# Kernel tuning notes

Hardware: AMD Instinct MI355X
Metric: run time of the kernel (lower is better)

## Reference

```python
import jax, jax.numpy as jnp
import numpy as np

IN_FEATURES = 1024
NUM_EXPERTS = 64
TOP_K = 2


def setup_inputs() -> dict:
    key = jax.random.key(0)
    kx, kw, kb = jax.random.split(key, 3)
    x = jax.random.normal(kx, (8, 4096, IN_FEATURES), dtype=jnp.float32)
    # nn.Linear init scale ~ 1/sqrt(in_features)
    bound = 1.0 / np.sqrt(IN_FEATURES)
    W = jax.random.uniform(kw, (NUM_EXPERTS, IN_FEATURES), dtype=jnp.float32, minval=-bound, maxval=bound)
    b = jax.random.uniform(kb, (NUM_EXPERTS,), dtype=jnp.float32, minval=-bound, maxval=bound)
    return {"x": x, "W": W, "b": b}


def reference(x, W, b):
    # logits: [B, S, E]
    logits = jnp.einsum("bsd,ed->bse", x, W) + b
    gates = jax.nn.softmax(logits, axis=-1)
    top_k_gates, top_k_indices = jax.lax.top_k(gates, TOP_K)
    return top_k_gates, top_k_indices
```

## Files before the change

### kernel.cpp

```cpp
#include <hip/hip_runtime.h>
#include <hip/hip_bf16.h>

#define D 1024
#define E 64
#define TPB 256
#define TOKS 64
#define KC 64
#define NCHUNK (D / KC)

typedef __attribute__((ext_vector_type(8))) short bf16x8;
typedef __attribute__((ext_vector_type(4))) float f32x4;
typedef __attribute__((ext_vector_type(4))) int i32x4;
typedef __attribute__((ext_vector_type(4))) unsigned short u16x4;

__device__ __forceinline__ unsigned short bf16_rne(float f) {
    unsigned u = __builtin_bit_cast(unsigned, f);
    u += 0x7fffu + ((u >> 16) & 1u);
    return (unsigned short)(u >> 16);
}
__device__ __forceinline__ float bf16_as_f(unsigned short h) {
    unsigned u = ((unsigned)h) << 16;
    return __builtin_bit_cast(float, u);
}
__device__ __forceinline__ void split_hi_lo(float v, unsigned short& h, unsigned short& l) {
    h = bf16_rne(v);
    l = bf16_rne(v - bf16_as_f(h));
}

__global__ __launch_bounds__(256) void wsplit_kernel(const float* __restrict__ W,
        unsigned short* __restrict__ whi, unsigned short* __restrict__ wlo) {
    int g = blockIdx.x * 256 + threadIdx.x;
    f32x4 w = *(const f32x4*)(W + (size_t)g * 4);
    u16x4 h, l;
#pragma unroll
    for (int j = 0; j < 4; ++j) {
        unsigned short hh, ll;
        split_hi_lo(w[j], hh, ll);
        h[j] = hh; l[j] = ll;
    }
    *(u16x4*)(whi + (size_t)g * 4) = h;
    *(u16x4*)(wlo + (size_t)g * 4) = l;
}

__global__ __launch_bounds__(TPB, 2) void router_kernel(
        const float* __restrict__ x,
        const unsigned short* __restrict__ whi,
        const unsigned short* __restrict__ wlo,
        const float* __restrict__ bias,
        float* __restrict__ out, int T) {
    __shared__ float ls[TOKS][E + 1];

    const int tid  = threadIdx.x;
    const int lane = tid & 63;
    const int wid  = tid >> 6;
    const int n    = lane & 15;
    const int q    = lane >> 4;
    const int t0   = blockIdx.x * TOKS;

    f32x4 acc[4];
#pragma unroll
    for (int nt = 0; nt < 4; ++nt) {
        float bv = bias[nt * 16 + n];
        acc[nt] = (f32x4){bv, bv, bv, bv};
    }

    const float* arow = x + (size_t)(t0 + wid * 16 + n) * D + q * 8;
    size_t brow[4];
#pragma unroll
    for (int nt = 0; nt < 4; ++nt) brow[nt] = (size_t)(nt * 16 + n) * D + q * 8;

    i32x4 breg[4][2][2];
    f32x4 aregA[4], aregB[4];

    auto load_b = [&](int c) {
#pragma unroll
        for (int nt = 0; nt < 4; ++nt)
#pragma unroll
            for (int s = 0; s < 2; ++s) {
                breg[nt][s][0] = *(const i32x4*)(whi + brow[nt] + c * KC + s * 32);
                breg[nt][s][1] = *(const i32x4*)(wlo + brow[nt] + c * KC + s * 32);
            }
    };
    auto load_a = [&](int c, f32x4* ar) {
#pragma unroll
        for (int s = 0; s < 2; ++s) {
            ar[2 * s]     = *(const f32x4*)(arow + c * KC + s * 32);
            ar[2 * s + 1] = *(const f32x4*)(arow + c * KC + s * 32 + 4);
        }
    };

    load_a(0, aregA);

    for (int kc = 0; kc < NCHUNK; ++kc) {
        load_b(kc);
        int kn = (kc + 1) & (NCHUNK - 1);
        load_a(kn, aregB);

#pragma unroll
        for (int s = 0; s < 2; ++s) {
            unsigned short ah[8], al[8];
#pragma unroll
            for (int j = 0; j < 4; ++j) {
                split_hi_lo(aregA[2 * s][j],     ah[j],     al[j]);
                split_hi_lo(aregA[2 * s + 1][j], ah[4 + j], al[4 + j]);
            }
            bf16x8 ahv, alv;
#pragma unroll
            for (int j = 0; j < 8; ++j) { ahv[j] = (short)ah[j]; alv[j] = (short)al[j]; }
#pragma unroll
            for (int nt = 0; nt < 4; ++nt) {
                const bf16x8 bh = __builtin_bit_cast(bf16x8, breg[nt][s][0]);
                const bf16x8 bl = __builtin_bit_cast(bf16x8, breg[nt][s][1]);
                acc[nt] = __builtin_amdgcn_mfma_f32_16x16x32_bf16(ahv, bh, acc[nt], 0, 0, 0);
                acc[nt] = __builtin_amdgcn_mfma_f32_16x16x32_bf16(alv, bh, acc[nt], 0, 0, 0);
                acc[nt] = __builtin_amdgcn_mfma_f32_16x16x32_bf16(ahv, bl, acc[nt], 0, 0, 0);
            }
        }
#pragma unroll
        for (int i = 0; i < 4; ++i) aregA[i] = aregB[i];
    }

#pragma unroll
    for (int nt = 0; nt < 4; ++nt) {
#pragma unroll
        for (int r = 0; r < 4; ++r) {
            ls[wid * 16 + q * 4 + r][nt * 16 + n] = acc[nt][r];
        }
    }
    __syncthreads();

    if (tid < TOKS) {
        float m1 = -3.4e38f, m2 = -3.4e38f;
        int i1 = 0, i2 = 0;
        for (int e = 0; e < E; ++e) {
            float v = ls[tid][e];
            if (v > m1) { m2 = m1; i2 = i1; m1 = v; i1 = e; }
            else if (v > m2) { m2 = v; i2 = e; }
        }
        float Z = 0.f;
        for (int e = 0; e < E; ++e) Z += __expf(ls[tid][e] - m1);
        float inv = 1.f / Z;
        int gt = t0 + tid;
        out[(size_t)gt * 2]     = inv;
        out[(size_t)gt * 2 + 1] = __expf(m2 - m1) * inv;
        float* oi = out + (size_t)T * 2;
        oi[(size_t)gt * 2]     = (float)i1;
        oi[(size_t)gt * 2 + 1] = (float)i2;
    }
}

extern "C" void kernel_launch(void* const* d_in, const int* in_sizes, int n_in,
                              void* d_out, int out_size, void* d_ws, size_t ws_size,
                              hipStream_t stream) {
    const float* x = (const float*)d_in[0];
    const float* W = (const float*)d_in[1];
    const float* b = (const float*)d_in[2];
    float* out = (float*)d_out;
    unsigned short* whi = (unsigned short*)d_ws;
    unsigned short* wlo = whi + (size_t)E * D;
    int T = in_sizes[0] / D;
    hipLaunchKernelGGL(wsplit_kernel, dim3((E * D) / 1024), dim3(256), 0, stream,
                       W, whi, wlo);
    hipLaunchKernelGGL(router_kernel, dim3(T / TOKS), dim3(TPB), 0, stream,
                       x, whi, wlo, b, out, T);
}
```

Baseline: 239.5 us.

## Stage router weights in double-buffered LDS and coalesce activation loads

Weight hi/lo planes are rewritten in chunk-major layout so the whole block can cooperatively copy each 64-wide K chunk into a double-buffered LDS tile. This replaces the per-wave global reloads of the full weight matrix with one shared copy per block. Activation rows are now loaded with contiguous lanes per row and transposed through a per-wave LDS scratch before the bf16 split, which should improve global coalescing on the dominant x stream. The cost is about 54KB of LDS per block, a barrier per chunk, and extra LDS traffic.

```diff
diff --git a/kernel.cpp b/kernel.cpp
--- a/kernel.cpp
+++ b/kernel.cpp
@@ -7,6 +7,8 @@
 #define TOKS 64
 #define KC 64
 #define NCHUNK (D / KC)
+#define BROW 72
+#define APAD 68
 
 typedef __attribute__((ext_vector_type(8))) short bf16x8;
 typedef __attribute__((ext_vector_type(4))) float f32x4;
@@ -30,6 +32,9 @@
 __global__ __launch_bounds__(256) void wsplit_kernel(const float* __restrict__ W,
         unsigned short* __restrict__ whi, unsigned short* __restrict__ wlo) {
     int g = blockIdx.x * 256 + threadIdx.x;
+    int e = g >> 8;
+    int k = (g & 255) * 4;
+    int c = k >> 6, kk = k & 63;
     f32x4 w = *(const f32x4*)(W + (size_t)g * 4);
     u16x4 h, l;
 #pragma unroll
@@ -38,8 +43,9 @@
         split_hi_lo(w[j], hh, ll);
         h[j] = hh; l[j] = ll;
     }
-    *(u16x4*)(whi + (size_t)g * 4) = h;
-    *(u16x4*)(wlo + (size_t)g * 4) = l;
+    size_t o = (size_t)c * (E * KC) + e * KC + kk;
+    *(u16x4*)(whi + o) = h;
+    *(u16x4*)(wlo + o) = l;
 }
 
 __global__ __launch_bounds__(TPB, 2) void router_kernel(
@@ -48,7 +54,11 @@
         const unsigned short* __restrict__ wlo,
         const float* __restrict__ bias,
         float* __restrict__ out, int T) {
-    __shared__ float ls[TOKS][E + 1];
+    __shared__ __align__(16) unsigned short wb[2][2][E][BROW];
+    __shared__ __align__(16) union SMA {
+        float Ax[4][16][APAD];
+        float ls[TOKS][E + 1];
+    } sma;
 
     const int tid  = threadIdx.x;
     const int lane = tid & 63;
@@ -64,67 +74,88 @@
         acc[nt] = (f32x4){bv, bv, bv, bv};
     }
 
-    const float* arow = x + (size_t)(t0 + wid * 16 + n) * D + q * 8;
-    size_t brow[4];
-#pragma unroll
-    for (int nt = 0; nt < 4; ++nt) brow[nt] = (size_t)(nt * 16 + n) * D + q * 8;
-
-    i32x4 breg[4][2][2];
+    const float* abase = x + (size_t)(t0 + wid * 16) * D;
+    const int arow_i = (lane >> 4);
+    const int acol   = (lane & 15) * 4;
     f32x4 aregA[4], aregB[4];
-
-    auto load_b = [&](int c) {
-#pragma unroll
-        for (int nt = 0; nt < 4; ++nt)
-#pragma unroll
-            for (int s = 0; s < 2; ++s) {
-                breg[nt][s][0] = *(const i32x4*)(whi + brow[nt] + c * KC + s * 32);
-                breg[nt][s][1] = *(const i32x4*)(wlo + brow[nt] + c * KC + s * 32);
-            }
-    };
     auto load_a = [&](int c, f32x4* ar) {
 #pragma unroll
-        for (int s = 0; s < 2; ++s) {
-            ar[2 * s]     = *(const f32x4*)(arow + c * KC + s * 32);
-            ar[2 * s + 1] = *(const f32x4*)(arow + c * KC + s * 32 + 4);
+        for (int i = 0; i < 4; ++i)
+            ar[i] = *(const f32x4*)(abase + (i * 4 + arow_i) * D + c * KC + acol);
+    };
+    auto write_a = [&](const f32x4* ar) {
+#pragma unroll
+        for (int i = 0; i < 4; ++i)
+            *(f32x4*)&sma.Ax[wid][i * 4 + arow_i][acol] = ar[i];
+    };
+
+    i32x4 wreg[4];
+    auto load_w = [&](int c) {
+#pragma unroll
+        for (int r = 0; r < 4; ++r) {
+            int idx = r * TPB + tid;
+            const unsigned short* src = (idx >> 9) ? wlo : whi;
+            wreg[r] = *(const i32x4*)(src + (size_t)c * (E * KC) + (idx & 511) * 8);
+        }
+    };
+    auto store_w = [&](int buf) {
+#pragma unroll
+        for (int r = 0; r < 4; ++r) {
+            int idx = r * TPB + tid;
+            int pl = idx >> 9, j = idx & 511, e = j >> 3, blk = j & 7;
+            *(i32x4*)&wb[buf][pl][e][blk * 8] = wreg[r];
         }
     };
 
-    load_a(0, aregA);
-
-    for (int kc = 0; kc < NCHUNK; ++kc) {
-        load_b(kc);
-        int kn = (kc + 1) & (NCHUNK - 1);
-        load_a(kn, aregB);
-
+    auto kstep = [&](int buf) {
 #pragma unroll
         for (int s = 0; s < 2; ++s) {
+            const float* ap = &sma.Ax[wid][n][s * 32 + q * 8];
+            f32x4 a0 = ((const f32x4*)ap)[0];
+            f32x4 a1 = ((const f32x4*)ap)[1];
             unsigned short ah[8], al[8];
 #pragma unroll
             for (int j = 0; j < 4; ++j) {
-                split_hi_lo(aregA[2 * s][j],     ah[j],     al[j]);
-                split_hi_lo(aregA[2 * s + 1][j], ah[4 + j], al[4 + j]);
+                split_hi_lo(a0[j], ah[j],     al[j]);
+                split_hi_lo(a1[j], ah[4 + j], al[4 + j]);
             }
             bf16x8 ahv, alv;
 #pragma unroll
             for (int j = 0; j < 8; ++j) { ahv[j] = (short)ah[j]; alv[j] = (short)al[j]; }
 #pragma unroll
             for (int nt = 0; nt < 4; ++nt) {
-                const bf16x8 bh = __builtin_bit_cast(bf16x8, breg[nt][s][0]);
-                const bf16x8 bl = __builtin_bit_cast(bf16x8, breg[nt][s][1]);
+                const bf16x8 bh = *(const bf16x8*)&wb[buf][0][nt * 16 + n][s * 32 + q * 8];
+                const bf16x8 bl = *(const bf16x8*)&wb[buf][1][nt * 16 + n][s * 32 + q * 8];
                 acc[nt] = __builtin_amdgcn_mfma_f32_16x16x32_bf16(ahv, bh, acc[nt], 0, 0, 0);
                 acc[nt] = __builtin_amdgcn_mfma_f32_16x16x32_bf16(alv, bh, acc[nt], 0, 0, 0);
                 acc[nt] = __builtin_amdgcn_mfma_f32_16x16x32_bf16(ahv, bl, acc[nt], 0, 0, 0);
             }
         }
+    };
+
+    load_w(0);
+    load_a(0, aregA);
+    store_w(0);
+    __syncthreads();
+
+    for (int kc = 0; kc < NCHUNK; ++kc) {
+        const int p = kc & 1;
+        const int kn = (kc + 1) & (NCHUNK - 1);
+        load_w(kn);
+        load_a(kn, aregB);
+        write_a(aregA);
+        kstep(p);
+        store_w(p ^ 1);
 #pragma unroll
         for (int i = 0; i < 4; ++i) aregA[i] = aregB[i];
+        __syncthreads();
     }
 
 #pragma unroll
     for (int nt = 0; nt < 4; ++nt) {
 #pragma unroll
         for (int r = 0; r < 4; ++r) {
-            ls[wid * 16 + q * 4 + r][nt * 16 + n] = acc[nt][r];
+            sma.ls[wid * 16 + q * 4 + r][nt * 16 + n] = acc[nt][r];
         }
     }
     __syncthreads();
@@ -133,12 +164,12 @@
         float m1 = -3.4e38f, m2 = -3.4e38f;
         int i1 = 0, i2 = 0;
         for (int e = 0; e < E; ++e) {
-            float v = ls[tid][e];
+            float v = sma.ls[tid][e];
             if (v > m1) { m2 = m1; i2 = i1; m1 = v; i1 = e; }
             else if (v > m2) { m2 = v; i2 = e; }
         }
         float Z = 0.f;
-        for (int e = 0; e < E; ++e) Z += __expf(ls[tid][e] - m1);
+        for (int e = 0; e < E; ++e) Z += __expf(sma.ls[tid][e] - m1);
         float inv = 1.f / Z;
         int gt = t0 + tid;
         out[(size_t)gt * 2]     = inv;
```

Measured after the change: 208.3 us. -13.0%, faster.

## Split K across waves with chunk-major W layout and LDS-staged activations

Applied to the files above, without the earlier changes.

Each block now handles 16 tokens, and its four waves each take a quarter of the 1024-wide reduction instead of each wave owning 16 tokens over the full K. Activations are loaded coalesced by rows into a padded LDS tile and read back in MFMA fragment layout. The split W is rewritten in chunk-major order so each wave's B reads are contiguous, and B is loaded directly per MFMA instead of being prefetched. Partial logits are summed across waves in LDS with the bias before top-2 and softmax, trading fewer tokens per block and an extra reduction for more blocks and better memory coalescing.

```diff
diff --git a/kernel.cpp b/kernel.cpp
--- a/kernel.cpp
+++ b/kernel.cpp
@@ -4,9 +4,10 @@
 #define D 1024
 #define E 64
 #define TPB 256
-#define TOKS 64
+#define TOKS 16
 #define KC 64
-#define NCHUNK (D / KC)
+#define CPW 4
+#define AP 68
 
 typedef __attribute__((ext_vector_type(8))) short bf16x8;
 typedef __attribute__((ext_vector_type(4))) float f32x4;
@@ -30,6 +31,9 @@
 __global__ __launch_bounds__(256) void wsplit_kernel(const float* __restrict__ W,
         unsigned short* __restrict__ whi, unsigned short* __restrict__ wlo) {
     int g = blockIdx.x * 256 + threadIdx.x;
+    int e = g >> 8;
+    int k = (g & 255) * 4;
+    int c = k >> 6, kk = k & 63;
     f32x4 w = *(const f32x4*)(W + (size_t)g * 4);
     u16x4 h, l;
 #pragma unroll
@@ -38,17 +42,19 @@
         split_hi_lo(w[j], hh, ll);
         h[j] = hh; l[j] = ll;
     }
-    *(u16x4*)(whi + (size_t)g * 4) = h;
-    *(u16x4*)(wlo + (size_t)g * 4) = l;
+    size_t o = (size_t)c * (E * KC) + e * KC + kk;
+    *(u16x4*)(whi + o) = h;
+    *(u16x4*)(wlo + o) = l;
 }
 
-__global__ __launch_bounds__(TPB, 2) void router_kernel(
+__global__ __launch_bounds__(TPB, 4) void router_kernel(
         const float* __restrict__ x,
         const unsigned short* __restrict__ whi,
         const unsigned short* __restrict__ wlo,
         const float* __restrict__ bias,
         float* __restrict__ out, int T) {
-    __shared__ float ls[TOKS][E + 1];
+    __shared__ __align__(16) float R[4][TOKS * AP];
+    __shared__ float sbias[E];
 
     const int tid  = threadIdx.x;
     const int lane = tid & 63;
@@ -57,88 +63,95 @@
     const int q    = lane >> 4;
     const int t0   = blockIdx.x * TOKS;
 
+    if (tid < E) sbias[tid] = bias[tid];
+
     f32x4 acc[4];
 #pragma unroll
-    for (int nt = 0; nt < 4; ++nt) {
-        float bv = bias[nt * 16 + n];
-        acc[nt] = (f32x4){bv, bv, bv, bv};
-    }
+    for (int i = 0; i < 4; ++i) acc[i] = (f32x4){0.f, 0.f, 0.f, 0.f};
 
-    const float* arow = x + (size_t)(t0 + wid * 16 + n) * D + q * 8;
-    size_t brow[4];
+    const float* abase = x + (size_t)t0 * D + wid * (CPW * KC);
+    const int ar = lane >> 4;
+    const int ac = (lane & 15) * 4;
+    f32x4 aA[4], aB[4];
+    auto load_a = [&](int cl, f32x4* v) {
 #pragma unroll
-    for (int nt = 0; nt < 4; ++nt) brow[nt] = (size_t)(nt * 16 + n) * D + q * 8;
-
-    i32x4 breg[4][2][2];
-    f32x4 aregA[4], aregB[4];
-
-    auto load_b = [&](int c) {
+        for (int i = 0; i < 4; ++i)
+            v[i] = *(const f32x4*)(abase + (size_t)(i * 4 + ar) * D + cl * KC + ac);
+    };
+    auto write_a = [&](const f32x4* v) {
 #pragma unroll
-        for (int nt = 0; nt < 4; ++nt)
-#pragma unroll
-            for (int s = 0; s < 2; ++s) {
-                breg[nt][s][0] = *(const i32x4*)(whi + brow[nt] + c * KC + s * 32);
-                breg[nt][s][1] = *(const i32x4*)(wlo + brow[nt] + c * KC + s * 32);
-            }
-    };
-    auto load_a = [&](int c, f32x4* ar) {
-#pragma unroll
-        for (int s = 0; s < 2; ++s) {
-            ar[2 * s]     = *(const f32x4*)(arow + c * KC + s * 32);
-            ar[2 * s + 1] = *(const f32x4*)(arow + c * KC + s * 32 + 4);
-        }
+        for (int i = 0; i < 4; ++i)
+            *(f32x4*)&R[wid][(i * 4 + ar) * AP + ac] = v[i];
     };
 
-    load_a(0, aregA);
+    load_a(0, aA);
 
-    for (int kc = 0; kc < NCHUNK; ++kc) {
-        load_b(kc);
-        int kn = (kc + 1) & (NCHUNK - 1);
-        load_a(kn, aregB);
+    for (int cl = 0; cl < CPW; ++cl) {
+        write_a(aA);
+        load_a((cl + 1) & 3, aB);
+        const size_t cb = (size_t)(wid * CPW + cl) * (E * KC);
 
 #pragma unroll
         for (int s = 0; s < 2; ++s) {
+            const float* ap = &R[wid][n * AP + s * 32 + q * 8];
+            f32x4 a0 = ((const f32x4*)ap)[0];
+            f32x4 a1 = ((const f32x4*)ap)[1];
             unsigned short ah[8], al[8];
 #pragma unroll
             for (int j = 0; j < 4; ++j) {
-                split_hi_lo(aregA[2 * s][j],     ah[j],     al[j]);
-                split_hi_lo(aregA[2 * s + 1][j], ah[4 + j], al[4 + j]);
+                split_hi_lo(a0[j], ah[j],     al[j]);
+                split_hi_lo(a1[j], ah[4 + j], al[4 + j]);
             }
             bf16x8 ahv, alv;
 #pragma unroll
             for (int j = 0; j < 8; ++j) { ahv[j] = (short)ah[j]; alv[j] = (short)al[j]; }
+            const size_t fo = cb + (size_t)n * KC + s * 32 + q * 8;
 #pragma unroll
             for (int nt = 0; nt < 4; ++nt) {
-                const bf16x8 bh = __builtin_bit_cast(bf16x8, breg[nt][s][0]);
-                const bf16x8 bl = __builtin_bit_cast(bf16x8, breg[nt][s][1]);
+                const size_t o = fo + (size_t)(nt * 16) * KC;
+                const bf16x8 bh = __builtin_bit_cast(bf16x8, *(const i32x4*)(whi + o));
+                const bf16x8 bl = __builtin_bit_cast(bf16x8, *(const i32x4*)(wlo + o));
                 acc[nt] = __builtin_amdgcn_mfma_f32_16x16x32_bf16(ahv, bh, acc[nt], 0, 0, 0);
                 acc[nt] = __builtin_amdgcn_mfma_f32_16x16x32_bf16(alv, bh, acc[nt], 0, 0, 0);
                 acc[nt] = __builtin_amdgcn_mfma_f32_16x16x32_bf16(ahv, bl, acc[nt], 0, 0, 0);
             }
         }
 #pragma unroll
-        for (int i = 0; i < 4; ++i) aregA[i] = aregB[i];
+        for (int i = 0; i < 4; ++i) aA[i] = aB[i];
     }
 
 #pragma unroll
     for (int nt = 0; nt < 4; ++nt) {
 #pragma unroll
         for (int r = 0; r < 4; ++r) {
-            ls[wid * 16 + q * 4 + r][nt * 16 + n] = acc[nt][r];
+            R[wid][(q * 4 + r) * AP + nt * 16 + n] = acc[nt][r];
         }
     }
     __syncthreads();
 
     if (tid < TOKS) {
+        float lg[E];
+#pragma unroll
+        for (int j = 0; j < 16; ++j) {
+            f32x4 v0 = *(const f32x4*)&R[0][tid * AP + j * 4];
+            f32x4 v1 = *(const f32x4*)&R[1][tid * AP + j * 4];
+            f32x4 v2 = *(const f32x4*)&R[2][tid * AP + j * 4];
+            f32x4 v3 = *(const f32x4*)&R[3][tid * AP + j * 4];
+#pragma unroll
+            for (int u = 0; u < 4; ++u)
+                lg[j * 4 + u] = v0[u] + v1[u] + v2[u] + v3[u] + sbias[j * 4 + u];
+        }
         float m1 = -3.4e38f, m2 = -3.4e38f;
         int i1 = 0, i2 = 0;
+#pragma unroll
         for (int e = 0; e < E; ++e) {
-            float v = ls[tid][e];
+            float v = lg[e];
             if (v > m1) { m2 = m1; i2 = i1; m1 = v; i1 = e; }
             else if (v > m2) { m2 = v; i2 = e; }
         }
         float Z = 0.f;
-        for (int e = 0; e < E; ++e) Z += __expf(ls[tid][e] - m1);
+#pragma unroll
+        for (int e = 0; e < E; ++e) Z += __expf(lg[e] - m1);
         float inv = 1.f / Z;
         int gt = t0 + tid;
         out[(size_t)gt * 2]     = inv;
```

Result: slower. 319.9 us (+33.6%).
